# Kernel optimization log

Measured on AMD Instinct MI355X. Metric: run time of the kernel, lower is better.

## Reference

```python
import jax, jax.numpy as jnp
import numpy as np

NEG = -1e9  # finite stand-in for -inf mask fill (scores are bounded by |v|_1)


def sparsemax(z):
    """Sparsemax over last axis (Martins & Astudillo 2016)."""
    zs = jnp.sort(z, axis=-1)[..., ::-1]                      # descending
    cs = jnp.cumsum(zs, axis=-1)
    k = jnp.arange(1, z.shape[-1] + 1, dtype=z.dtype)
    support = 1.0 + k * zs > cs
    ksz = jnp.sum(support, axis=-1, keepdims=True)            # support size >= 1
    cs_k = jnp.take_along_axis(cs, ksz.astype(jnp.int32) - 1, axis=-1)
    tau = (cs_k - 1.0) / ksz.astype(z.dtype)
    return jnp.maximum(z - tau, 0.0)


def bahdanau_head(query, values, mask, Wk, Wq, v):
    # query: [B,1,H], values: [B,S,K], mask: [B,1,S]
    proj_keys = values @ Wk                                   # [B,S,H] (precomputed keys)
    proj_q = query @ Wq                                       # [B,1,H]
    scores = jnp.einsum('bsh,h->bs', jnp.tanh(proj_q + proj_keys), v)[:, None, :]  # [B,1,S]
    scores = jnp.where(mask, scores, NEG)
    alphas = sparsemax(scores)                                # [B,1,S]
    context = alphas @ values                                 # [B,1,K]
    return context, alphas


def setup_inputs() -> dict:
    B, S, K, H = 32, 4096, 512, 512
    key = jax.random.key(0)
    ks = jax.random.split(key, 16)
    sc = lambda d: 1.0 / np.sqrt(d)
    mk = lambda k, shp: (jax.random.uniform(k, shp) < 0.95).at[..., 0].set(True)
    return {
        'query': jax.random.normal(ks[0], (B, 1, H), jnp.float32),
        'values_a': jax.random.normal(ks[1], (B, S, K), jnp.float32),
        'values_b': jax.random.normal(ks[2], (B, S, K), jnp.float32),
        'mask_a': mk(ks[3], (B, 1, S)),
        'mask_b': mk(ks[4], (B, 1, S)),
        'Wk_a': jax.random.normal(ks[5], (K, H), jnp.float32) * sc(K),
        'Wq_a': jax.random.normal(ks[6], (H, H), jnp.float32) * sc(H),
        'v_a': jax.random.normal(ks[7], (H,), jnp.float32) * sc(H),
        'Wk_b': jax.random.normal(ks[8], (K, H), jnp.float32) * sc(K),
        'Wq_b': jax.random.normal(ks[9], (H, H), jnp.float32) * sc(H),
        'v_b': jax.random.normal(ks[10], (H,), jnp.float32) * sc(H),
        'Wg': jax.random.normal(ks[11], (H + 2 * K, 2), jnp.float32) * sc(H + 2 * K),
        'bg': jnp.zeros((2,), jnp.float32),
        'Wu_a': jax.random.normal(ks[12], (K + H, H), jnp.float32) * sc(K + H),
        'bu_a': jnp.zeros((H,), jnp.float32),
        'Wu_b': jax.random.normal(ks[13], (K + H, H), jnp.float32) * sc(K + H),
        'bu_b': jnp.zeros((H,), jnp.float32),
    }


def reference(query, values_a, values_b, mask_a, mask_b,
              Wk_a, Wq_a, v_a, Wk_b, Wq_b, v_b,
              Wg, bg, Wu_a, bu_a, Wu_b, bu_b):
    ctx_a, al_a = bahdanau_head(query, values_a, mask_a, Wk_a, Wq_a, v_a)
    ctx_b, al_b = bahdanau_head(query, values_b, mask_b, Wk_b, Wq_b, v_b)
    # AttentionGate merge
    gate_in = jnp.concatenate([query, ctx_a, ctx_b], axis=2)          # [B,1,H+2K]
    gate_w = jax.nn.softmax(gate_in @ Wg + bg, axis=-1)               # [B,1,2]
    cand_a = jnp.tanh(jnp.concatenate([query, ctx_a], axis=2) @ Wu_a + bu_a)  # [B,1,H]
    cand_b = jnp.tanh(jnp.concatenate([query, ctx_b], axis=2) @ Wu_b + bu_b)
    cands = jnp.concatenate([cand_a, cand_b], axis=1)                 # [B,2,H]
    att_vector = gate_w @ cands                                       # [B,1,H]
    return att_vector, al_a, al_b
```

## Files before the change

### kernel.cpp

```cpp
#include <hip/hip_runtime.h>
#include <math.h>

#define NEGV (-1e9f)
constexpr int B = 32, S = 4096, K = 512, H = 512;

typedef __attribute__((ext_vector_type(8))) short bf16x8;
typedef __attribute__((ext_vector_type(4))) float f32x4;

__device__ __forceinline__ short f2bf(float x) {
  union { float f; unsigned u; } v; v.f = x;
  unsigned r = (v.u + 0x7FFFu + ((v.u >> 16) & 1u)) >> 16;
  return (short)r;
}

__device__ __forceinline__ float fast_tanh(float x) {
  return 1.f - 2.f / (__expf(2.f * x) + 1.f);
}

__global__ __launch_bounds__(64)
void wkswizzle_kernel(const float* __restrict__ Wk_a, const float* __restrict__ Wk_b,
                      short* __restrict__ WkT) {
  const int head = blockIdx.y;
  const float* __restrict__ Wk = head ? Wk_b : Wk_a;
  const int cn = blockIdx.x;
  const int c = cn >> 5, n = cn & 31;
  const int l = threadIdx.x;
  const int kb = c * 32 + ((l >> 4) << 3);
  const int h = n * 16 + (l & 15);
  bf16x8 frag;
#pragma unroll
  for (int j = 0; j < 8; ++j) frag[j] = f2bf(Wk[(size_t)(kb + j) * H + h]);
  *(bf16x8*)(WkT + (size_t)head * 262144 + ((size_t)cn * 64 + l) * 8) = frag;
}

__global__ __launch_bounds__(512)
void qproj_kernel(const float* __restrict__ query,
                  const float* __restrict__ Wq_a,
                  const float* __restrict__ Wq_b,
                  float* __restrict__ qproj) {
  const int b = blockIdx.x, head = blockIdx.y;
  const float* __restrict__ Wq = head ? Wq_b : Wq_a;
  __shared__ float qs[H];
  qs[threadIdx.x] = query[b * H + threadIdx.x];
  __syncthreads();
  const int h = threadIdx.x;
  float acc = 0.f;
#pragma unroll 8
  for (int k = 0; k < H; ++k) acc = fmaf(qs[k], Wq[k * H + h], acc);
  qproj[(head * B + b) * H + h] = acc;
}

__global__ __launch_bounds__(256, 4)
void scores_mfma_kernel(const float* __restrict__ values_a, const float* __restrict__ values_b,
                        const short* __restrict__ WkT,
                        const float* __restrict__ v_a, const float* __restrict__ v_b,
                        const float* __restrict__ qproj,
                        float* __restrict__ scores_part) {
  const int head = blockIdx.z, b = blockIdx.y;
  const int s0 = (blockIdx.x >> 1) * 64;
  const int hslab = blockIdx.x & 1;
  const float* __restrict__ V  = (head ? values_b : values_a) + (size_t)b * S * K;
  const float* __restrict__ v  = head ? v_b : v_a;
  const float* __restrict__ qp = qproj + (head * B + b) * H;
  const short* __restrict__ wkb = WkT + (size_t)head * 262144;

  __shared__ __align__(16) short Albuf[2][4 * 64 * 8];
  __shared__ float red[4 * 64];

  const int tid = threadIdx.x;
  const int w = tid >> 6, l = tid & 63;

  const int sa = tid >> 2, ka = (tid & 3) * 8;
  const float* const arow = V + (size_t)(s0 + sa) * K + ka;
  const int afrag = (sa >> 4) * 64 + ((sa & 15) | ((ka >> 3) << 4));
  const short* const bbase = wkb + ((size_t)(hslab * 16 + w * 4) * 64 + l) * 8;

  f32x4 acc[4][4] = {};

  float4 p0 = *(const float4*)(arow);
  float4 p1 = *(const float4*)(arow + 4);
  {
    bf16x8 af;
    af[0] = f2bf(p0.x); af[1] = f2bf(p0.y); af[2] = f2bf(p0.z); af[3] = f2bf(p0.w);
    af[4] = f2bf(p1.x); af[5] = f2bf(p1.y); af[6] = f2bf(p1.z); af[7] = f2bf(p1.w);
    *(bf16x8*)(Albuf[0] + afrag * 8) = af;
  }
  int pb = 0;
  for (int c = 0; c < 16; ++c) {
    if (c < 15) {
      p0 = *(const float4*)(arow + (c + 1) * 32);
      p1 = *(const float4*)(arow + (c + 1) * 32 + 4);
    }
    bf16x8 bfr[4];
#pragma unroll
    for (int nl = 0; nl < 4; ++nl)
      bfr[nl] = *(const bf16x8*)(bbase + ((size_t)c * 32 + nl) * 512);
    __syncthreads();
    bf16x8 afr[4];
#pragma unroll
    for (int i = 0; i < 4; ++i) afr[i] = *(const bf16x8*)(Albuf[pb] + (i * 64 + l) * 8);
#pragma unroll
    for (int nl = 0; nl < 4; ++nl)
#pragma unroll
      for (int i = 0; i < 4; ++i)
        acc[i][nl] = __builtin_amdgcn_mfma_f32_16x16x32_bf16(afr[i], bfr[nl], acc[i][nl], 0, 0, 0);
    if (c < 15) {
      bf16x8 af;
      af[0] = f2bf(p0.x); af[1] = f2bf(p0.y); af[2] = f2bf(p0.z); af[3] = f2bf(p0.w);
      af[4] = f2bf(p1.x); af[5] = f2bf(p1.y); af[6] = f2bf(p1.z); af[7] = f2bf(p1.w);
      *(bf16x8*)(Albuf[pb ^ 1] + afrag * 8) = af;
      pb ^= 1;
    }
  }

  float qpr[4], vr[4];
#pragma unroll
  for (int nl = 0; nl < 4; ++nl) {
    const int h = (hslab * 16 + w * 4 + nl) * 16 + (l & 15);
    qpr[nl] = qp[h];
    vr[nl] = v[h];
  }
#pragma unroll
  for (int i = 0; i < 4; ++i)
#pragma unroll
    for (int r = 0; r < 4; ++r) {
      float p = 0.f;
#pragma unroll
      for (int nl = 0; nl < 4; ++nl) p = fmaf(vr[nl], fast_tanh(acc[i][nl][r] + qpr[nl]), p);
#pragma unroll
      for (int off = 8; off > 0; off >>= 1) p += __shfl_xor(p, off, 64);
      if ((l & 15) == 0) red[w * 64 + i * 16 + (l >> 4) * 4 + r] = p;
    }
  __syncthreads();
  if (tid < 64) {
    const float tot = red[tid] + red[64 + tid] + red[128 + tid] + red[192 + tid];
    scores_part[(((size_t)hslab * 2 + head) * B + b) * S + s0 + tid] = tot;
  }
}

__device__ __forceinline__ float bred256(float v, const bool is_max, float* lds) {
#pragma unroll
  for (int o = 32; o > 0; o >>= 1) {
    const float t = __shfl_xor(v, o, 64);
    v = is_max ? fmaxf(v, t) : (v + t);
  }
  __syncthreads();
  if ((threadIdx.x & 63) == 0) lds[threadIdx.x >> 6] = v;
  __syncthreads();
  return is_max ? fmaxf(fmaxf(lds[0], lds[1]), fmaxf(lds[2], lds[3]))
                : (lds[0] + lds[1]) + (lds[2] + lds[3]);
}

__global__ __launch_bounds__(256)
void sparsemax_kernel(const float* __restrict__ scores_part,
                      const int* __restrict__ mask_a, const int* __restrict__ mask_b,
                      float* __restrict__ d_out_f) {
  const int b = blockIdx.x, head = blockIdx.y;
  const float* __restrict__ z0 = scores_part + (((size_t)0 * 2 + head) * B + b) * S;
  const float* __restrict__ z1 = scores_part + (((size_t)1 * 2 + head) * B + b) * S;
  const int* __restrict__ mask = (head ? mask_b : mask_a) + b * S;
  float* __restrict__ alpha = d_out_f + B * H + (size_t)head * B * S + (size_t)b * S;
  __shared__ float lds[4];
  const int tid = threadIdx.x;
  float e[16];
#pragma unroll
  for (int t = 0; t < 16; ++t) {
    const int s = t * 256 + tid;
    e[t] = mask[s] ? (z0[s] + z1[s]) : NEGV;
  }
  float m = NEGV;
#pragma unroll
  for (int t = 0; t < 16; ++t) m = fmaxf(m, e[t]);
  m = bred256(m, true, lds);
  float lo = m - 1.f, hi = m;
  for (int it = 0; it < 28; ++it) {
    const float mid = 0.5f * (lo + hi);
    float s = 0.f;
#pragma unroll
    for (int t = 0; t < 16; ++t) s += fmaxf(e[t] - mid, 0.f);
    s = bred256(s, false, lds);
    if (s >= 1.f) lo = mid; else hi = mid;
  }
  float cnt = 0.f, sum = 0.f;
#pragma unroll
  for (int t = 0; t < 16; ++t) {
    if (e[t] > lo) { cnt += 1.f; sum += e[t]; }
  }
  cnt = bred256(cnt, false, lds);
  sum = bred256(sum, false, lds);
  const float tau = (sum - 1.f) / cnt;
#pragma unroll
  for (int t = 0; t < 16; ++t) alpha[t * 256 + tid] = fmaxf(e[t] - tau, 0.f);
}

__global__ __launch_bounds__(512)
void context_kernel(const float* __restrict__ values_a, const float* __restrict__ values_b,
                    const float* __restrict__ d_out_f, float* __restrict__ ctx) {
  const int b = blockIdx.x, head = blockIdx.y;
  const float* __restrict__ V = (head ? values_b : values_a) + (size_t)b * S * K;
  const float* __restrict__ al = d_out_f + B * H + (size_t)head * B * S + (size_t)b * S;
  __shared__ int cnt;
  __shared__ int sidx[S];
  __shared__ float sal[S];
  if (threadIdx.x == 0) cnt = 0;
  __syncthreads();
  for (int i = threadIdx.x; i < S; i += 512) {
    const float a = al[i];
    if (a > 0.f) { const int p = atomicAdd(&cnt, 1); sidx[p] = i; sal[p] = a; }
  }
  __syncthreads();
  const int n = cnt;
  const int j = threadIdx.x;
  float acc = 0.f;
  for (int t = 0; t < n; ++t) acc = fmaf(sal[t], V[(size_t)sidx[t] * K + j], acc);
  ctx[(head * B + b) * K + j] = acc;
}

__global__ __launch_bounds__(512)
void merge_kernel(const float* __restrict__ query, const float* __restrict__ ctx,
                  const float* __restrict__ Wg, const float* __restrict__ bg,
                  const float* __restrict__ Wu_a, const float* __restrict__ bu_a,
                  const float* __restrict__ Wu_b, const float* __restrict__ bu_b,
                  float* __restrict__ att) {
  const int b = blockIdx.x;
  __shared__ float gin[1536];
  __shared__ float lred[16];
  __shared__ float gw[2];
  const int tid = threadIdx.x;
  gin[tid]        = query[b * H + tid];
  gin[512 + tid]  = ctx[(0 * B + b) * K + tid];
  gin[1024 + tid] = ctx[(1 * B + b) * K + tid];
  __syncthreads();
  float p0 = 0.f, p1 = 0.f;
  for (int i = tid; i < 1536; i += 512) {
    const float x = gin[i];
    p0 = fmaf(x, Wg[i * 2 + 0], p0);
    p1 = fmaf(x, Wg[i * 2 + 1], p1);
  }
#pragma unroll
  for (int o = 32; o > 0; o >>= 1) { p0 += __shfl_xor(p0, o, 64); p1 += __shfl_xor(p1, o, 64); }
  if ((tid & 63) == 0) { lred[tid >> 6] = p0; lred[8 + (tid >> 6)] = p1; }
  __syncthreads();
  if (tid == 0) {
    float l0 = bg[0], l1 = bg[1];
    for (int w = 0; w < 8; ++w) { l0 += lred[w]; l1 += lred[8 + w]; }
    const float mx = fmaxf(l0, l1);
    const float e0 = expf(l0 - mx), e1 = expf(l1 - mx);
    gw[0] = e0 / (e0 + e1);
    gw[1] = e1 / (e0 + e1);
  }
  __syncthreads();
  const int h = tid;
  float aa = bu_a[h], ab = bu_b[h];
  for (int i = 0; i < 1024; ++i) aa = fmaf(gin[i], Wu_a[i * H + h], aa);
  for (int i = 0; i < 1024; ++i) {
    const float x = (i < 512) ? gin[i] : gin[i + 512];
    ab = fmaf(x, Wu_b[i * H + h], ab);
  }
  att[b * H + h] = gw[0] * tanhf(aa) + gw[1] * tanhf(ab);
}

extern "C" void kernel_launch(void* const* d_in, const int* in_sizes, int n_in,
                              void* d_out, int out_size, void* d_ws, size_t ws_size,
                              hipStream_t stream) {
  const float* query    = (const float*)d_in[0];
  const float* values_a = (const float*)d_in[1];
  const float* values_b = (const float*)d_in[2];
  const int*   mask_a   = (const int*)d_in[3];
  const int*   mask_b   = (const int*)d_in[4];
  const float* Wk_a = (const float*)d_in[5];
  const float* Wq_a = (const float*)d_in[6];
  const float* v_a  = (const float*)d_in[7];
  const float* Wk_b = (const float*)d_in[8];
  const float* Wq_b = (const float*)d_in[9];
  const float* v_b  = (const float*)d_in[10];
  const float* Wg   = (const float*)d_in[11];
  const float* bg   = (const float*)d_in[12];
  const float* Wu_a = (const float*)d_in[13];
  const float* bu_a = (const float*)d_in[14];
  const float* Wu_b = (const float*)d_in[15];
  const float* bu_b = (const float*)d_in[16];
  float* out = (float*)d_out;

  float* wsf         = (float*)d_ws;
  float* qproj       = wsf;
  float* scores_part = wsf + 2 * B * H;
  float* ctx         = wsf + 2 * B * H + 4 * B * S;
  short* WkT         = (short*)(wsf + 2 * B * H + 4 * B * S + 2 * B * K);

  wkswizzle_kernel<<<dim3(512, 2), 64, 0, stream>>>(Wk_a, Wk_b, WkT);
  qproj_kernel<<<dim3(B, 2), 512, 0, stream>>>(query, Wq_a, Wq_b, qproj);
  scores_mfma_kernel<<<dim3(128, B, 2), 256, 0, stream>>>(
      values_a, values_b, WkT, v_a, v_b, qproj, scores_part);
  sparsemax_kernel<<<dim3(B, 2), 256, 0, stream>>>(scores_part, mask_a, mask_b, out);
  context_kernel<<<dim3(B, 2), 512, 0, stream>>>(values_a, values_b, out, ctx);
  merge_kernel<<<B, 512, 0, stream>>>(query, ctx, Wg, bg, Wu_a, bu_a, Wu_b, bu_b, out);
}
```

Measured before the change: 889.9 us.

## Merge H-slab split into one 512-thread block per S tile, packed bf16 convert

Each scores block now computes all 512 hidden units for a 64-row S tile with 8 waves, instead of two blocks each covering half of H. This avoids reading and converting the values tile twice and removes the partial-score buffer and its summation in sparsemax. The K loop now steps 64 per iteration with deeper register prefetch, and uses the packed hardware bf16 conversion instruction. The cost is fewer blocks and higher register and LDS pressure per block, which may reduce occupancy.

```diff
diff --git a/kernel.cpp b/kernel.cpp
--- a/kernel.cpp
+++ b/kernel.cpp
@@ -6,11 +6,27 @@
 
 typedef __attribute__((ext_vector_type(8))) short bf16x8;
 typedef __attribute__((ext_vector_type(4))) float f32x4;
+typedef __attribute__((ext_vector_type(4))) int i32x4;
 
 __device__ __forceinline__ short f2bf(float x) {
   union { float f; unsigned u; } v; v.f = x;
   unsigned r = (v.u + 0x7FFFu + ((v.u >> 16) & 1u)) >> 16;
   return (short)r;
+}
+
+__device__ __forceinline__ unsigned cvt_pk_bf16(float lo, float hi) {
+  unsigned r;
+  asm("v_cvt_pk_bf16_f32 %0, %1, %2" : "=v"(r) : "v"(lo), "v"(hi));
+  return r;
+}
+
+__device__ __forceinline__ void cvt_store16(short* dst, const float4 a, const float4 b) {
+  i32x4 t;
+  t[0] = (int)cvt_pk_bf16(a.x, a.y);
+  t[1] = (int)cvt_pk_bf16(a.z, a.w);
+  t[2] = (int)cvt_pk_bf16(b.x, b.y);
+  t[3] = (int)cvt_pk_bf16(b.z, b.w);
+  *(i32x4*)dst = t;
 }
 
 __device__ __forceinline__ float fast_tanh(float x) {
@@ -50,73 +66,71 @@
   qproj[(head * B + b) * H + h] = acc;
 }
 
-__global__ __launch_bounds__(256, 4)
+__global__ __launch_bounds__(512, 2)
 void scores_mfma_kernel(const float* __restrict__ values_a, const float* __restrict__ values_b,
                         const short* __restrict__ WkT,
                         const float* __restrict__ v_a, const float* __restrict__ v_b,
                         const float* __restrict__ qproj,
-                        float* __restrict__ scores_part) {
+                        float* __restrict__ scores) {
   const int head = blockIdx.z, b = blockIdx.y;
-  const int s0 = (blockIdx.x >> 1) * 64;
-  const int hslab = blockIdx.x & 1;
+  const int s0 = blockIdx.x * 64;
   const float* __restrict__ V  = (head ? values_b : values_a) + (size_t)b * S * K;
   const float* __restrict__ v  = head ? v_b : v_a;
   const float* __restrict__ qp = qproj + (head * B + b) * H;
   const short* __restrict__ wkb = WkT + (size_t)head * 262144;
 
-  __shared__ __align__(16) short Albuf[2][4 * 64 * 8];
-  __shared__ float red[4 * 64];
+  __shared__ __align__(16) short Albuf[2][4096];
+  __shared__ float red[8 * 64];
 
   const int tid = threadIdx.x;
   const int w = tid >> 6, l = tid & 63;
 
-  const int sa = tid >> 2, ka = (tid & 3) * 8;
+  const int sa = tid >> 3, ka = (tid & 7) * 8;
   const float* const arow = V + (size_t)(s0 + sa) * K + ka;
-  const int afrag = (sa >> 4) * 64 + ((sa & 15) | ((ka >> 3) << 4));
-  const short* const bbase = wkb + ((size_t)(hslab * 16 + w * 4) * 64 + l) * 8;
+  const int aline = (((ka >> 5) * 4 + (sa >> 4)) * 64 + ((sa & 15) | (((ka & 31) >> 3) << 4))) * 8;
+  const short* const bbase = wkb + ((w * 4) * 64 + l) * 8;
 
   f32x4 acc[4][4] = {};
 
-  float4 p0 = *(const float4*)(arow);
-  float4 p1 = *(const float4*)(arow + 4);
-  {
-    bf16x8 af;
-    af[0] = f2bf(p0.x); af[1] = f2bf(p0.y); af[2] = f2bf(p0.z); af[3] = f2bf(p0.w);
-    af[4] = f2bf(p1.x); af[5] = f2bf(p1.y); af[6] = f2bf(p1.z); af[7] = f2bf(p1.w);
-    *(bf16x8*)(Albuf[0] + afrag * 8) = af;
-  }
-  int pb = 0;
-  for (int c = 0; c < 16; ++c) {
-    if (c < 15) {
-      p0 = *(const float4*)(arow + (c + 1) * 32);
-      p1 = *(const float4*)(arow + (c + 1) * 32 + 4);
+  float4 pfa[2], pfb[2];
+  pfa[0] = *(const float4*)(arow);
+  pfb[0] = *(const float4*)(arow + 4);
+  pfa[1] = *(const float4*)(arow + 64);
+  pfb[1] = *(const float4*)(arow + 68);
+  cvt_store16(&Albuf[0][aline], pfa[0], pfb[0]);
+
+#pragma unroll
+  for (int c = 0; c < 8; ++c) {
+    bf16x8 bfr[2][4];
+#pragma unroll
+    for (int kk = 0; kk < 2; ++kk)
+#pragma unroll
+      for (int nl = 0; nl < 4; ++nl)
+        bfr[kk][nl] = *(const bf16x8*)(bbase + ((2 * c + kk) * 32 + nl) * 512);
+    if (c < 6) {
+      pfa[c & 1] = *(const float4*)(arow + (c + 2) * 64);
+      pfb[c & 1] = *(const float4*)(arow + (c + 2) * 64 + 4);
     }
-    bf16x8 bfr[4];
-#pragma unroll
-    for (int nl = 0; nl < 4; ++nl)
-      bfr[nl] = *(const bf16x8*)(bbase + ((size_t)c * 32 + nl) * 512);
     __syncthreads();
-    bf16x8 afr[4];
-#pragma unroll
-    for (int i = 0; i < 4; ++i) afr[i] = *(const bf16x8*)(Albuf[pb] + (i * 64 + l) * 8);
-#pragma unroll
-    for (int nl = 0; nl < 4; ++nl)
+#pragma unroll
+    for (int kk = 0; kk < 2; ++kk) {
+      bf16x8 afr[4];
 #pragma unroll
       for (int i = 0; i < 4; ++i)
-        acc[i][nl] = __builtin_amdgcn_mfma_f32_16x16x32_bf16(afr[i], bfr[nl], acc[i][nl], 0, 0, 0);
-    if (c < 15) {
-      bf16x8 af;
-      af[0] = f2bf(p0.x); af[1] = f2bf(p0.y); af[2] = f2bf(p0.z); af[3] = f2bf(p0.w);
-      af[4] = f2bf(p1.x); af[5] = f2bf(p1.y); af[6] = f2bf(p1.z); af[7] = f2bf(p1.w);
-      *(bf16x8*)(Albuf[pb ^ 1] + afrag * 8) = af;
-      pb ^= 1;
+        afr[i] = *(const bf16x8*)(&Albuf[c & 1][((kk * 4 + i) * 64 + l) * 8]);
+#pragma unroll
+      for (int nl = 0; nl < 4; ++nl)
+#pragma unroll
+        for (int i = 0; i < 4; ++i)
+          acc[i][nl] = __builtin_amdgcn_mfma_f32_16x16x32_bf16(afr[i], bfr[kk][nl], acc[i][nl], 0, 0, 0);
     }
+    if (c < 7) cvt_store16(&Albuf[(c & 1) ^ 1][aline], pfa[(c + 1) & 1], pfb[(c + 1) & 1]);
   }
 
   float qpr[4], vr[4];
 #pragma unroll
   for (int nl = 0; nl < 4; ++nl) {
-    const int h = (hslab * 16 + w * 4 + nl) * 16 + (l & 15);
+    const int h = (w * 4 + nl) * 16 + (l & 15);
     qpr[nl] = qp[h];
     vr[nl] = v[h];
   }
@@ -133,8 +147,10 @@
     }
   __syncthreads();
   if (tid < 64) {
-    const float tot = red[tid] + red[64 + tid] + red[128 + tid] + red[192 + tid];
-    scores_part[(((size_t)hslab * 2 + head) * B + b) * S + s0 + tid] = tot;
+    float tot = 0.f;
+#pragma unroll
+    for (int ww = 0; ww < 8; ++ww) tot += red[ww * 64 + tid];
+    scores[((size_t)head * B + b) * S + s0 + tid] = tot;
   }
 }
 
@@ -152,12 +168,11 @@
 }
 
 __global__ __launch_bounds__(256)
-void sparsemax_kernel(const float* __restrict__ scores_part,
+void sparsemax_kernel(const float* __restrict__ scores,
                       const int* __restrict__ mask_a, const int* __restrict__ mask_b,
                       float* __restrict__ d_out_f) {
   const int b = blockIdx.x, head = blockIdx.y;
-  const float* __restrict__ z0 = scores_part + (((size_t)0 * 2 + head) * B + b) * S;
-  const float* __restrict__ z1 = scores_part + (((size_t)1 * 2 + head) * B + b) * S;
+  const float* __restrict__ z = scores + ((size_t)head * B + b) * S;
   const int* __restrict__ mask = (head ? mask_b : mask_a) + b * S;
   float* __restrict__ alpha = d_out_f + B * H + (size_t)head * B * S + (size_t)b * S;
   __shared__ float lds[4];
@@ -166,7 +181,7 @@
 #pragma unroll
   for (int t = 0; t < 16; ++t) {
     const int s = t * 256 + tid;
-    e[t] = mask[s] ? (z0[s] + z1[s]) : NEGV;
+    e[t] = mask[s] ? z[s] : NEGV;
   }
   float m = NEGV;
 #pragma unroll
@@ -282,17 +297,17 @@
   const float* bu_b = (const float*)d_in[16];
   float* out = (float*)d_out;
 
-  float* wsf         = (float*)d_ws;
-  float* qproj       = wsf;
-  float* scores_part = wsf + 2 * B * H;
-  float* ctx         = wsf + 2 * B * H + 4 * B * S;
-  short* WkT         = (short*)(wsf + 2 * B * H + 4 * B * S + 2 * B * K);
+  float* wsf    = (float*)d_ws;
+  float* qproj  = wsf;
+  float* scores = wsf + 2 * B * H;
+  float* ctx    = wsf + 2 * B * H + 2 * B * S;
+  short* WkT    = (short*)(wsf + 2 * B * H + 2 * B * S + 2 * B * K);
 
   wkswizzle_kernel<<<dim3(512, 2), 64, 0, stream>>>(Wk_a, Wk_b, WkT);
   qproj_kernel<<<dim3(B, 2), 512, 0, stream>>>(query, Wq_a, Wq_b, qproj);
-  scores_mfma_kernel<<<dim3(128, B, 2), 256, 0, stream>>>(
-      values_a, values_b, WkT, v_a, v_b, qproj, scores_part);
-  sparsemax_kernel<<<dim3(B, 2), 256, 0, stream>>>(scores_part, mask_a, mask_b, out);
+  scores_mfma_kernel<<<dim3(S / 64, B, 2), 512, 0, stream>>>(
+      values_a, values_b, WkT, v_a, v_b, qproj, scores);
+  sparsemax_kernel<<<dim3(B, 2), 256, 0, stream>>>(scores, mask_a, mask_b, out);
   context_kernel<<<dim3(B, 2), 512, 0, stream>>>(values_a, values_b, out, ctx);
   merge_kernel<<<B, 512, 0, stream>>>(query, ctx, Wg, bg, Wu_a, bu_a, Wu_b, bu_b, out);
 }
```

Result: faster. 846.6 us (-4.9%).

## Tune scores MFMA loop: hw bf16 pack, LDS swizzle, block remap, lighter barriers

Applied to the files above, without the earlier changes.

Replaces the software bf16 rounding with the v_cvt_pk_bf16_f32 instruction and writes A fragments through an XOR-swizzled LDS layout to cut bank conflicts. It also remaps block indices so consecutive blocks spread across heads, batches and s-tiles, which changes L2/cache locality. The loop is fully unrolled, uses an lgkmcnt-only barrier instead of __syncthreads, and raises wave priority around the MFMA block. The risks are rounding differences from the hardware conversion and higher register pressure from unrolling.

```diff
diff --git a/kernel.cpp b/kernel.cpp
--- a/kernel.cpp
+++ b/kernel.cpp
@@ -6,6 +6,7 @@
 
 typedef __attribute__((ext_vector_type(8))) short bf16x8;
 typedef __attribute__((ext_vector_type(4))) float f32x4;
+typedef __attribute__((ext_vector_type(4))) int i32x4;
 
 __device__ __forceinline__ short f2bf(float x) {
   union { float f; unsigned u; } v; v.f = x;
@@ -13,8 +14,29 @@
   return (short)r;
 }
 
+__device__ __forceinline__ unsigned cvt_pk_bf16(float lo, float hi) {
+  unsigned r;
+  asm("v_cvt_pk_bf16_f32 %0, %1, %2" : "=v"(r) : "v"(lo), "v"(hi));
+  return r;
+}
+
+__device__ __forceinline__ void cvt_store16(short* dst, const float4 a, const float4 b) {
+  i32x4 t;
+  t[0] = (int)cvt_pk_bf16(a.x, a.y);
+  t[1] = (int)cvt_pk_bf16(a.z, a.w);
+  t[2] = (int)cvt_pk_bf16(b.x, b.y);
+  t[3] = (int)cvt_pk_bf16(b.z, b.w);
+  *(i32x4*)dst = t;
+}
+
 __device__ __forceinline__ float fast_tanh(float x) {
   return 1.f - 2.f / (__expf(2.f * x) + 1.f);
+}
+
+__device__ __forceinline__ void block_sync_lds() {
+  asm volatile("s_waitcnt lgkmcnt(0)" ::: "memory");
+  __builtin_amdgcn_s_barrier();
+  __builtin_amdgcn_sched_barrier(0);
 }
 
 __global__ __launch_bounds__(64)
@@ -56,60 +78,61 @@
                         const float* __restrict__ v_a, const float* __restrict__ v_b,
                         const float* __restrict__ qproj,
                         float* __restrict__ scores_part) {
-  const int head = blockIdx.z, b = blockIdx.y;
-  const int s0 = (blockIdx.x >> 1) * 64;
-  const int hslab = blockIdx.x & 1;
+  const int lin = blockIdx.x + 128 * (blockIdx.y + 32 * blockIdx.z);
+  const int wk = ((lin & 7) << 10) | (lin >> 3);
+  const int hslab = wk & 1;
+  const int s0 = ((wk >> 1) & 63) * 64;
+  const int b = (wk >> 7) & 31;
+  const int head = (wk >> 12) & 1;
+
   const float* __restrict__ V  = (head ? values_b : values_a) + (size_t)b * S * K;
   const float* __restrict__ v  = head ? v_b : v_a;
   const float* __restrict__ qp = qproj + (head * B + b) * H;
   const short* __restrict__ wkb = WkT + (size_t)head * 262144;
 
-  __shared__ __align__(16) short Albuf[2][4 * 64 * 8];
+  __shared__ __align__(16) short Albuf[2][2048];
   __shared__ float red[4 * 64];
 
   const int tid = threadIdx.x;
   const int w = tid >> 6, l = tid & 63;
 
-  const int sa = tid >> 2, ka = (tid & 3) * 8;
-  const float* const arow = V + (size_t)(s0 + sa) * K + ka;
-  const int afrag = (sa >> 4) * 64 + ((sa & 15) | ((ka >> 3) << 4));
+  const int sa = tid >> 2, g = tid & 3;
+  const float* const arow = V + (size_t)(s0 + sa) * K + g * 8;
+  const int Lw = (((sa >> 4) * 64) + ((sa & 15) | (g << 4))) ^ g;
+  const int rs = l ^ (l >> 4);
   const short* const bbase = wkb + ((size_t)(hslab * 16 + w * 4) * 64 + l) * 8;
 
   f32x4 acc[4][4] = {};
 
   float4 p0 = *(const float4*)(arow);
   float4 p1 = *(const float4*)(arow + 4);
-  {
-    bf16x8 af;
-    af[0] = f2bf(p0.x); af[1] = f2bf(p0.y); af[2] = f2bf(p0.z); af[3] = f2bf(p0.w);
-    af[4] = f2bf(p1.x); af[5] = f2bf(p1.y); af[6] = f2bf(p1.z); af[7] = f2bf(p1.w);
-    *(bf16x8*)(Albuf[0] + afrag * 8) = af;
-  }
-  int pb = 0;
+  cvt_store16(&Albuf[0][Lw * 8], p0, p1);
+  block_sync_lds();
+
+#pragma unroll
   for (int c = 0; c < 16; ++c) {
+    bf16x8 bfr[4];
+#pragma unroll
+    for (int nl = 0; nl < 4; ++nl)
+      bfr[nl] = *(const bf16x8*)(bbase + ((size_t)(c * 32 + nl)) * 512);
     if (c < 15) {
       p0 = *(const float4*)(arow + (c + 1) * 32);
       p1 = *(const float4*)(arow + (c + 1) * 32 + 4);
     }
-    bf16x8 bfr[4];
-#pragma unroll
-    for (int nl = 0; nl < 4; ++nl)
-      bfr[nl] = *(const bf16x8*)(bbase + ((size_t)c * 32 + nl) * 512);
-    __syncthreads();
     bf16x8 afr[4];
 #pragma unroll
-    for (int i = 0; i < 4; ++i) afr[i] = *(const bf16x8*)(Albuf[pb] + (i * 64 + l) * 8);
+    for (int i = 0; i < 4; ++i)
+      afr[i] = *(const bf16x8*)(&Albuf[c & 1][(i * 64 + rs) * 8]);
+    __builtin_amdgcn_s_setprio(1);
 #pragma unroll
     for (int nl = 0; nl < 4; ++nl)
 #pragma unroll
       for (int i = 0; i < 4; ++i)
         acc[i][nl] = __builtin_amdgcn_mfma_f32_16x16x32_bf16(afr[i], bfr[nl], acc[i][nl], 0, 0, 0);
+    __builtin_amdgcn_s_setprio(0);
     if (c < 15) {
-      bf16x8 af;
-      af[0] = f2bf(p0.x); af[1] = f2bf(p0.y); af[2] = f2bf(p0.z); af[3] = f2bf(p0.w);
-      af[4] = f2bf(p1.x); af[5] = f2bf(p1.y); af[6] = f2bf(p1.z); af[7] = f2bf(p1.w);
-      *(bf16x8*)(Albuf[pb ^ 1] + afrag * 8) = af;
-      pb ^= 1;
+      cvt_store16(&Albuf[(c & 1) ^ 1][Lw * 8], p0, p1);
+      block_sync_lds();
     }
   }
 
```

Result: faster. 813.0 us (-8.6%).
